# Performance work log

Measured on AMD Instinct MI355X. Metric: run time of the kernel, lower is better.

## Reference

```python
import jax, jax.numpy as jnp
import numpy as np

N_NODES = 400
HID = 96
DEC = 64
FEAT_STATIC = 8
FEAT = FEAT_STATIC + N_NODES  # 408
EPS = 1e-8


def prelu(x, a):
    # single-parameter PReLU (torch default num_parameters=1)
    return jnp.where(x >= 0, x, a * x)


def setup_inputs() -> dict:
    key = jax.random.key(0)
    ks = jax.random.split(key, 16)
    B = 16
    E = N_NODES * (N_NODES - 1) // 2  # 79800

    x = jax.random.normal(ks[0], (B, E), dtype=jnp.float32)
    node_features = jax.random.normal(ks[1], (B, N_NODES, FEAT_STATIC), dtype=jnp.float32)
    sc_matrix = jax.random.uniform(ks[2], (B, N_NODES, N_NODES), dtype=jnp.float32)

    # normalization buffers (computed from train split in torch; random stand-ins)
    static_mean = jax.random.normal(ks[3], (1, 1, FEAT_STATIC), dtype=jnp.float32) * 0.1
    static_std = jnp.ones((1, 1, FEAT_STATIC), dtype=jnp.float32)

    def lin(k, fin, fout):
        kw, kb = jax.random.split(k)
        lim = 1.0 / np.sqrt(fin)
        W = jax.random.uniform(kw, (fin, fout), minval=-lim, maxval=lim, dtype=jnp.float32)
        b = jax.random.uniform(kb, (fout,), minval=-lim, maxval=lim, dtype=jnp.float32)
        return W, b

    W_e1, b_e1 = lin(ks[4], FEAT, HID)
    W_e2, b_e2 = lin(ks[5], HID, HID)
    W_d1, b_d1 = lin(ks[6], 3 * HID, DEC)  # symmetric decoder: 3 * node_embed_dim
    W_d2, b_d2 = lin(ks[7], DEC, DEC)
    W_d3, b_d3 = lin(ks[8], DEC, 1)

    a25 = jnp.float32(0.25)

    ei_np, ej_np = np.triu_indices(N_NODES, k=1)
    ei = jnp.asarray(ei_np, dtype=jnp.int32)
    ej = jnp.asarray(ej_np, dtype=jnp.int32)

    return {
        "x": x, "node_features": node_features, "sc_matrix": sc_matrix,
        "static_mean": static_mean, "static_std": static_std,
        "W_e1": W_e1, "b_e1": b_e1, "a_e1": a25,
        "W_e2": W_e2, "b_e2": b_e2, "a_e2": a25,
        "W_d1": W_d1, "b_d1": b_d1, "a_d1": a25,
        "W_d2": W_d2, "b_d2": b_d2, "a_d2": a25,
        "W_d3": W_d3, "b_d3": b_d3,
        "ei": ei, "ej": ej,
    }


def reference(x, node_features, sc_matrix, static_mean, static_std,
              W_e1, b_e1, a_e1, W_e2, b_e2, a_e2,
              W_d1, b_d1, a_d1, W_d2, b_d2, a_d2, W_d3, b_d3, ei, ej):
    # x (SC upper triangle) is only used for batch size in the torch module.
    # static anatomical block: z-score with train stats
    s = (node_features - static_mean) / (static_std + EPS)  # [B,N,8]
    # sc_row block, 'brain_scale': divide by per-matrix mean
    m = sc_matrix / jnp.maximum(
        jnp.mean(sc_matrix, axis=(-2, -1), keepdims=True), EPS)  # [B,N,N]
    feats = jnp.concatenate([s, m], axis=-1)  # [B,N,408]

    # shared node encoder (dropout inactive at eval)
    h = prelu(feats @ W_e1 + b_e1, a_e1)
    h = prelu(h @ W_e2 + b_e2, a_e2)  # [B,N,96]

    # per-edge gather over upper-triangle indices
    h_i = h[:, ei, :]  # [B,E,96]
    h_j = h[:, ej, :]
    # symmetric edge features
    edge_feat = jnp.concatenate(
        [h_i + h_j, jnp.abs(h_i - h_j), h_i * h_j], axis=-1)  # [B,E,288]

    z = prelu(edge_feat @ W_d1 + b_d1, a_d1)
    z = prelu(z @ W_d2 + b_d2, a_d2)
    out = (z @ W_d3 + b_d3)[..., 0]  # [B,E]
    return out
```

## Files before the change

kernel.cpp:

```cpp
#include <hip/hip_runtime.h>

#define NN 400
#define HID 96
#define EDGES 79800
#define BATCH 16
#define ROWS (BATCH*EDGES)
#define NT 13
#define NPAIRS 91

typedef _Float16 f16;
typedef f16 f16x2 __attribute__((ext_vector_type(2)));
typedef f16 f16x8 __attribute__((ext_vector_type(8)));
typedef __fp16 fp16x2 __attribute__((ext_vector_type(2)));
typedef float f32x16 __attribute__((ext_vector_type(16)));
typedef unsigned int u32;
typedef unsigned long long u64;

union H8 { f16x8 h; u32 u[4]; f16x2 p[4]; fp16x2 q[4]; u64 d[2]; };
union C2 { f16x2 h; fp16x2 q; u32 u; };

__device__ inline f16x2 pkrtz(float a, float b) {
  C2 c; c.q = __builtin_amdgcn_cvt_pkrtz(a, b); return c.h;
}
__device__ inline u32 pkrtz_u(float a, float b) {
  C2 c; c.q = __builtin_amdgcn_cvt_pkrtz(a, b); return c.u;
}
__device__ inline float fdot2a(f16x2 a, f16x2 b, float c) {
#if __has_builtin(__builtin_amdgcn_fdot2)
  C2 ca, cb; ca.h = a; cb.h = b;
  return __builtin_amdgcn_fdot2(ca.q, cb.q, c, false);
#else
  return c + (float)a.x*(float)b.x + (float)a.y*(float)b.y;
#endif
}

__device__ inline f16x8 habs8(f16x8 x) {
  H8 t; t.h = x;
  t.u[0] &= 0x7fff7fffu; t.u[1] &= 0x7fff7fffu;
  t.u[2] &= 0x7fff7fffu; t.u[3] &= 0x7fff7fffu;
  return t.h;
}

__device__ inline f16x8 pack8(float a0,float a1,float a2,float a3,
                              float a4,float a5,float a6,float a7){
  H8 u;
  u.p[0] = pkrtz(a0,a1);
  u.p[1] = pkrtz(a2,a3);
  u.p[2] = pkrtz(a4,a5);
  u.p[3] = pkrtz(a6,a7);
  return u.h;
}

__global__ void prep_mean_kernel(const float* __restrict__ We1, const float* __restrict__ We2,
                                 const float* __restrict__ W1, const float* __restrict__ W2,
                                 const float* __restrict__ sc,
                                 u32* __restrict__ wq, float* __restrict__ mpart) {
  if (blockIdx.x >= 140) {
    int p = blockIdx.x - 140;
    int b = p >> 4, part = p & 15;
    const float4* src = (const float4*)(sc + (size_t)b*160000) + part*2500;
    float s = 0.f;
    for (int i = threadIdx.x; i < 2500; i += 256) {
      float4 v = src[i];
      s += (v.x + v.y) + (v.z + v.w);
    }
    __shared__ float red[256];
    red[threadIdx.x] = s; __syncthreads();
    for (int off = 128; off > 0; off >>= 1) {
      if (threadIdx.x < off) red[threadIdx.x] += red[threadIdx.x + off];
      __syncthreads();
    }
    if (threadIdx.x == 0) mpart[p] = red[0];
    return;
  }
  int D = blockIdx.x*256 + threadIdx.x;
  float v0, v1;
  if (D < 9216) {
    int frag = D >> 8;  int t = frag >> 1, q = frag & 1;
    int rem = D & 255;  int lane = rem >> 2, dj = rem & 3;
    int c = lane & 31, h2 = lane >> 5;
    int k = 16*t + 8*h2 + 2*dj;
    int d = 32*q + c;
    v0 = W1[k*64 + d]; v1 = W1[(k+1)*64 + d];
  } else if (D < 11264) {
    int Dl = D - 9216;
    int frag = Dl >> 8; int t2 = frag >> 1, q = frag & 1;
    int rem = Dl & 255; int lane = rem >> 2, dj = rem & 3;
    int c = lane & 31, h2 = lane >> 5;
    int p = 8*t2 + 4*h2 + dj;
    int d = 32*q + c;
    v0 = W2[p*64 + d]; v1 = W2[(p+32)*64 + d];
  } else if (D < 31232) {
    int Dl = D - 11264;
    int frag = Dl >> 8; int t = frag/3, ct = frag - 3*t;
    int rem = Dl & 255; int lane = rem >> 2, dj = rem & 3;
    int c = lane & 31, h2 = lane >> 5;
    int k0 = 16*t + 8*h2 + 2*dj, k1 = k0 + 1;
    int d = 32*ct + c;
    v0 = (k0 < 400) ? We1[(8+k0)*96 + d] : (k0 < 408 ? We1[(k0-400)*96 + d] : 0.f);
    v1 = (k1 < 400) ? We1[(8+k1)*96 + d] : (k1 < 408 ? We1[(k1-400)*96 + d] : 0.f);
  } else {
    int Dl = D - 31232;
    int frag = Dl >> 8; int t = frag/3, ct = frag - 3*t;
    int rem = Dl & 255; int lane = rem >> 2, dj = rem & 3;
    int c = lane & 31, h2 = lane >> 5;
    int k = 16*t + 8*h2 + 2*dj;
    int d = 32*ct + c;
    v0 = We2[k*96 + d]; v1 = We2[(k+1)*96 + d];
  }
  wq[D] = pkrtz_u(v0, v1);
}

__global__ __launch_bounds__(256) void enc_kernel(
    const float* __restrict__ sc, const float* __restrict__ nf,
    const float* __restrict__ smean, const float* __restrict__ sstd,
    const float* __restrict__ be1, const float* __restrict__ ae1,
    const float* __restrict__ be2, const float* __restrict__ ae2,
    const float* __restrict__ mpart, const u32* __restrict__ wq,
    f16* __restrict__ hout) {
  __shared__ u32 lds[12288 + 1664];
  const int tid = threadIdx.x;
  const int wid = tid >> 6, lane = tid & 63;
  const int c = lane & 31, h2 = lane >> 5;
  const int r0 = blockIdx.x * 32;
  {
    int row = tid >> 3, seg = tid & 7;
    int r = r0 + row;
    int b = r / 400;
    float ms = 0.f;
    const float4* mp4 = (const float4*)(mpart + 16*b);
#pragma unroll
    for (int k = 0; k < 4; ++k) { float4 v = mp4[k]; ms += (v.x+v.y)+(v.z+v.w); }
    float rm = 1.f / fmaxf(ms*(1.f/160000.f), 1e-8f);
    const float4* src = (const float4*)(sc + (size_t)r*400);
#pragma unroll
    for (int i = 0; i < 13; ++i) {
      int col4 = seg + 8*i;
      if (col4 < 100) {
        float4 v = src[col4];
        u32 lo = pkrtz_u(v.x*rm, v.y*rm);
        u32 hi = pkrtz_u(v.z*rm, v.w*rm);
        *(u64*)(lds + row*210 + col4*2) = (u64)lo | ((u64)hi << 32);
      }
    }
  }
  __syncthreads();
  int tb = (wid==0) ? 0 : (wid==1) ? 7 : (wid==2) ? 14 : 20;
  int te = (wid==0) ? 7 : (wid==1) ? 14 : (wid==2) ? 20 : 26;
  f32x16 acc[3] = {};
  const u32* wb1 = wq + 11264;
  for (int t = tb; t < te; ++t) {
    f16x8 af;
    if (t < 25) {
      H8 av;
      const u32* ap = lds + c*210 + 8*t + 4*h2;
      av.d[0] = *(const u64*)ap;
      av.d[1] = *(const u64*)(ap + 2);
      af = av.h;
    } else {
      af = (f16x8){};
      if (h2 == 0) {
        int r = r0 + c;
        float q0[8];
#pragma unroll
        for (int j = 0; j < 8; ++j)
          q0[j] = (nf[r*8 + j] - smean[j]) / (sstd[j] + 1e-8f);
        af = pack8(q0[0],q0[1],q0[2],q0[3],q0[4],q0[5],q0[6],q0[7]);
      }
    }
#pragma unroll
    for (int ct = 0; ct < 3; ++ct) {
      f16x8 bf = *(const f16x8*)(wb1 + ((t*3+ct)*64 + lane)*4);
      acc[ct] = __builtin_amdgcn_mfma_f32_32x32x16_f16(af, bf, acc[ct], 0,0,0);
    }
  }
  __syncthreads();
#pragma unroll
  for (int ct = 0; ct < 3; ++ct) {
    union { f32x16 v; float4 f[4]; } u; u.v = acc[ct];
#pragma unroll
    for (int i4 = 0; i4 < 4; ++i4)
      *(float4*)(lds + (((wid*3+ct)*4 + i4)*64 + lane)*4) = u.f[i4];
  }
  __syncthreads();
  f16* zb16 = (f16*)(lds + 12288);
  const float a1 = *ae1;
  if (wid < 3) {
    float bv = be1[32*wid + c];
    f32x16 s;
#pragma unroll
    for (int i = 0; i < 16; ++i) s[i] = bv;
#pragma unroll
    for (int w2 = 0; w2 < 4; ++w2) {
#pragma unroll
      for (int i4 = 0; i4 < 4; ++i4) {
        float4 f = *(const float4*)(lds + (((w2*3+wid)*4 + i4)*64 + lane)*4);
        s[4*i4+0] += f.x; s[4*i4+1] += f.y; s[4*i4+2] += f.z; s[4*i4+3] += f.w;
      }
    }
#pragma unroll
    for (int r = 0; r < 16; ++r) {
      float v = s[r]; v = fmaxf(v, a1*v);
      int row = (r & 3) + 8*(r >> 2) + 4*h2;
      zb16[row*104 + 32*wid + c] = (f16)v;
    }
  }
  __syncthreads();
  if (wid < 3) {
    const float a2 = *ae2;
    float bv = be2[32*wid + c];
    f32x16 acc2;
#pragma unroll
    for (int i = 0; i < 16; ++i) acc2[i] = bv;
    const u32* wb2 = wq + 31232;
#pragma unroll
    for (int t = 0; t < 6; ++t) {
      f16x8 af = *(const f16x8*)(zb16 + c*104 + 16*t + 8*h2);
      f16x8 bf = *(const f16x8*)(wb2 + ((t*3+wid)*64 + lane)*4);
      acc2 = __builtin_amdgcn_mfma_f32_32x32x16_f16(af, bf, acc2, 0,0,0);
    }
#pragma unroll
    for (int rr = 0; rr < 16; ++rr) {
      int row = (rr & 3) + 8*(rr >> 2) + 4*h2;
      float v = acc2[rr]; v = fmaxf(v, a2*v);
      hout[(r0 + row)*96 + 32*wid + c] = (f16)v;
    }
  }
}

__global__ __launch_bounds__(256, 2) void decoder_kernel(
    const f16* __restrict__ hbuf, const u32* __restrict__ wq,
    const float* __restrict__ b1, const float* __restrict__ b2,
    const float* __restrict__ ad1, const float* __restrict__ ad2,
    const float* __restrict__ W3, const float* __restrict__ b3p,
    float* __restrict__ out) {
  __shared__ alignas(16) u32 smem[15872];
  const int tid = threadIdx.x;
  int p = blockIdx.x;
  int b = p / NPAIRS, pr = p - b*NPAIRS;
  int I = 0;
  while (pr >= NT - I) { pr -= NT - I; ++I; }
  const int J = I + pr;
  {
    int r = tid >> 2;
    int side = r >> 5, rr = r & 31;
    int nb = (side ? J : I)*32 + rr;
    nb = nb < NN ? nb : NN-1;
    const float4* src = (const float4*)(hbuf + (size_t)(b*NN + nb)*HID) + (tid & 3)*3;
    float4* dst = (float4*)(smem + side*1536 + rr*48) + (tid & 3)*3;
    dst[0] = src[0]; dst[1] = src[1]; dst[2] = src[2];
  }
  {
    float4* dst = (float4*)(smem + 3072);
    const float4* srcw = (const float4*)wq;
    for (int i = tid; i < 2048; i += 256) dst[i] = srcw[i];
  }
  __syncthreads();

  const int lane = tid & 63;
  const int wid  = tid >> 6;
  const int c = lane & 31, h2 = lane >> 5;
  const f16* hI16 = (const f16*)smem;
  const f16* hJrow = (const f16*)(smem + 1536) + c*HID;
  const f16* wfr = (const f16*)(smem + 3072);
  u32* zb = smem + 11264 + wid*1152;
  f16x8 bp4[2], bp5[2];
  bp4[0] = *(const f16x8*)(wq + ((32+0)*64 + lane)*4);
  bp4[1] = *(const f16x8*)(wq + ((32+1)*64 + lane)*4);
  bp5[0] = *(const f16x8*)(wq + ((34+0)*64 + lane)*4);
  bp5[1] = *(const f16x8*)(wq + ((34+1)*64 + lane)*4);
  f16x8 w2f[4][2];
#pragma unroll
  for (int t2 = 0; t2 < 4; ++t2) {
    w2f[t2][0] = *(const f16x8*)(wq + 9216 + ((t2*2+0)*64 + lane)*4);
    w2f[t2][1] = *(const f16x8*)(wq + 9216 + ((t2*2+1)*64 + lane)*4);
  }
  const float b1x = b1[c], b1y = b1[c+32];
  const float b2x = b2[c], b2y = b2[c+32];
  const float a1 = *ad1, a2 = *ad2, b3 = *b3p;
  const f16x2 a1v = pkrtz(a1, a1);
  const f16x2 a2v = pkrtz(a2, a2);
  const f16x2 w3p = pkrtz(W3[c], W3[c+32]);
  const f16x2 ones2 = pkrtz(1.f, 1.f);
  const int gj = J*32 + c;
  const int bofs = b*EDGES;

  for (int it = 0; it < 4; ++it) {
    const int i0 = it*8 + wid*2;
    const f16* hi0 = hI16 + (i0+0)*HID;
    const f16* hi1 = hI16 + (i0+1)*HID;
    f32x16 acc[2][2];
#pragma unroll
    for (int r = 0; r < 16; ++r) {
      acc[0][0][r] = b1x; acc[0][1][r] = b1y;
      acc[1][0][r] = b1x; acc[1][1][r] = b1y;
    }
#pragma unroll
    for (int t = 0; t < 6; ++t) {
      f16x8 bs0 = *(const f16x8*)(wfr + (((t   )*2+0)*64 + lane)*8);
      f16x8 bs1 = *(const f16x8*)(wfr + (((t   )*2+1)*64 + lane)*8);
      f16x8 bd0 = *(const f16x8*)(wfr + (((t+ 6)*2+0)*64 + lane)*8);
      f16x8 bd1 = *(const f16x8*)(wfr + (((t+ 6)*2+1)*64 + lane)*8);
      f16x8 bp0 = (t < 4) ? *(const f16x8*)(wfr + (((t+12)*2+0)*64 + lane)*8)
                          : (t == 4 ? bp4[0] : bp5[0]);
      f16x8 bp1 = (t < 4) ? *(const f16x8*)(wfr + (((t+12)*2+1)*64 + lane)*8)
                          : (t == 4 ? bp4[1] : bp5[1]);
      f16x8 hj = *(const f16x8*)(hJrow + 16*t + 8*h2);
#pragma unroll
      for (int m = 0; m < 2; ++m) {
        f16x8 hi = *(const f16x8*)((m ? hi1 : hi0) + 16*t + 8*h2);
        f16x8 su = hi + hj;
        f16x8 di = habs8(hi - hj);
        f16x8 prd = hi * hj;
        acc[m][0] = __builtin_amdgcn_mfma_f32_32x32x16_f16(su, bs0, acc[m][0], 0,0,0);
        acc[m][1] = __builtin_amdgcn_mfma_f32_32x32x16_f16(su, bs1, acc[m][1], 0,0,0);
        acc[m][0] = __builtin_amdgcn_mfma_f32_32x32x16_f16(di, bd0, acc[m][0], 0,0,0);
        acc[m][1] = __builtin_amdgcn_mfma_f32_32x32x16_f16(di, bd1, acc[m][1], 0,0,0);
        acc[m][0] = __builtin_amdgcn_mfma_f32_32x32x16_f16(prd, bp0, acc[m][0], 0,0,0);
        acc[m][1] = __builtin_amdgcn_mfma_f32_32x32x16_f16(prd, bp1, acc[m][1], 0,0,0);
      }
    }
#pragma unroll
    for (int m = 0; m < 2; ++m) {
#pragma unroll
      for (int r = 0; r < 16; ++r) {
        f16x2 pz = pkrtz(acc[m][0][r], acc[m][1][r]);
        pz = __builtin_elementwise_max(pz, pz * a1v);
        C2 cv; cv.h = pz;
        int row = (r & 3) + 8*(r >> 2) + 4*h2;
        zb[row*36 + c] = cv.u;
      }
      f16x8 za[4];
#pragma unroll
      for (int t2 = 0; t2 < 4; ++t2)
        za[t2] = *(const f16x8*)((const f16*)zb + (c*36 + 8*t2 + 4*h2)*2);
      f32x16 zacc[2];
#pragma unroll
      for (int r = 0; r < 16; ++r) { zacc[0][r] = b2x; zacc[1][r] = b2y; }
#pragma unroll
      for (int t2 = 0; t2 < 4; ++t2) {
        zacc[0] = __builtin_amdgcn_mfma_f32_32x32x16_f16(za[t2], w2f[t2][0], zacc[0], 0,0,0);
        zacc[1] = __builtin_amdgcn_mfma_f32_32x32x16_f16(za[t2], w2f[t2][1], zacc[1], 0,0,0);
      }
#pragma unroll
      for (int r = 0; r < 16; ++r) {
        f16x2 pz = pkrtz(zacc[0][r], zacc[1][r]);
        pz = __builtin_elementwise_max(pz, pz * a2v);
        pz = pz * w3p;
        C2 cv; cv.h = pz;
        int row = (r & 3) + 8*(r >> 2) + 4*h2;
        zb[row*36 + c] = cv.u;
      }
      float ssum = 0.f;
#pragma unroll
      for (int g = 0; g < 4; ++g) {
        H8 v; v.h = *(const f16x8*)((const f16*)zb + (c*36 + 16*h2 + 4*g)*2);
#pragma unroll
        for (int dw = 0; dw < 4; ++dw)
          ssum = fdot2a(v.p[dw], ones2, ssum);
      }
      ssum += __shfl_xor(ssum, 32);
      int gi = I*32 + i0 + m;
      bool valid = (gi < gj) && (gj < NN);
      if (h2 == 0 && valid) {
        int eo = bofs + gi*(799 - gi)/2 + (gj - gi - 1);
        out[eo] = ssum + b3;
      }
    }
  }
}

extern "C" void kernel_launch(void* const* d_in, const int* in_sizes, int n_in,
                              void* d_out, int out_size, void* d_ws, size_t ws_size,
                              hipStream_t stream) {
  const float* nf  = (const float*)d_in[1];
  const float* sc  = (const float*)d_in[2];
  const float* sm  = (const float*)d_in[3];
  const float* ss  = (const float*)d_in[4];
  const float* We1 = (const float*)d_in[5];
  const float* be1 = (const float*)d_in[6];
  const float* ae1 = (const float*)d_in[7];
  const float* We2 = (const float*)d_in[8];
  const float* be2 = (const float*)d_in[9];
  const float* ae2 = (const float*)d_in[10];
  const float* W1  = (const float*)d_in[11];
  const float* b1  = (const float*)d_in[12];
  const float* a1  = (const float*)d_in[13];
  const float* W2  = (const float*)d_in[14];
  const float* b2  = (const float*)d_in[15];
  const float* a2  = (const float*)d_in[16];
  const float* W3  = (const float*)d_in[17];
  const float* b3  = (const float*)d_in[18];
  float* out = (float*)d_out;

  char* ws = (char*)d_ws;
  float* mpart = (float*)ws;
  f16*   hbuf = (f16*)(ws + 1024);
  u32*   wq   = (u32*)(ws + 1024 + 1228800);

  prep_mean_kernel<<<396, 256, 0, stream>>>(We1, We2, W1, W2, sc, wq, mpart);
  enc_kernel<<<200, 256, 0, stream>>>(sc, nf, sm, ss, be1, ae1, be2, ae2,
                                      mpart, wq, hbuf);
  decoder_kernel<<<BATCH*NPAIRS, 256, 0, stream>>>(hbuf, wq, b1, b2, a1, a2,
                                                   W3, b3, out);
}
```

Before: 184.7 us.

## Transpose decoder MFMAs to keep intermediates in registers via permlane32 swap

Swaps the MFMA operand roles so weights become the A operand and edge features the B operand. The layer-1 output then feeds layer 2 straight from registers using permlane32_swap, replacing the LDS round-trip through a per-wave z buffer. The layer-3 dot product is done in registers against prepacked W3 pairs. Biases are injected through an extra rank-1 MFMA, the J-side node rows are loaded directly into registers, and W2 moves into LDS. Shared memory shrinks, so launch bounds rise to 3 blocks per CU, at the cost of extra MFMAs and higher register pressure.

Measured after the change: 353.7 us. 91.5% more time.

```diff
diff --git a/kernel.cpp b/kernel.cpp
--- a/kernel.cpp
+++ b/kernel.cpp
@@ -49,6 +49,11 @@
   u.p[2] = pkrtz(a4,a5);
   u.p[3] = pkrtz(a6,a7);
   return u.h;
+}
+
+__device__ inline void plswap(u32 &x, u32 &y) {
+  auto r = __builtin_amdgcn_permlane32_swap((int)x, (int)y, false, false);
+  x = (u32)r[0]; y = (u32)r[1];
 }
 
 __global__ void prep_mean_kernel(const float* __restrict__ We1, const float* __restrict__ We2,
@@ -87,9 +92,9 @@
     int frag = Dl >> 8; int t2 = frag >> 1, q = frag & 1;
     int rem = Dl & 255; int lane = rem >> 2, dj = rem & 3;
     int c = lane & 31, h2 = lane >> 5;
-    int p = 8*t2 + 4*h2 + dj;
+    int k = 16*t2 + 8*h2 + 2*dj;
     int d = 32*q + c;
-    v0 = W2[p*64 + d]; v1 = W2[(p+32)*64 + d];
+    v0 = W2[k*64 + d]; v1 = W2[(k+1)*64 + d];
   } else if (D < 31232) {
     int Dl = D - 11264;
     int frag = Dl >> 8; int t = frag/3, ct = frag - 3*t;
@@ -228,141 +233,138 @@
   }
 }
 
-__global__ __launch_bounds__(256, 2) void decoder_kernel(
+__global__ __launch_bounds__(256, 3) void decoder_kernel(
     const f16* __restrict__ hbuf, const u32* __restrict__ wq,
     const float* __restrict__ b1, const float* __restrict__ b2,
     const float* __restrict__ ad1, const float* __restrict__ ad2,
     const float* __restrict__ W3, const float* __restrict__ b3p,
     float* __restrict__ out) {
-  __shared__ alignas(16) u32 smem[15872];
+  __shared__ alignas(16) u32 smem[12800];
   const int tid = threadIdx.x;
   int p = blockIdx.x;
   int b = p / NPAIRS, pr = p - b*NPAIRS;
   int I = 0;
   while (pr >= NT - I) { pr -= NT - I; ++I; }
   const int J = I + pr;
+  for (int i = tid; i < 384; i += 256) {
+    int row = i / 12, off = i - row*12;
+    int nb = I*32 + row; nb = nb < NN ? nb : NN-1;
+    const float4* src = (const float4*)(hbuf + (size_t)(b*NN + nb)*HID) + off;
+    *((float4*)(smem + row*48) + off) = *src;
+  }
   {
-    int r = tid >> 2;
-    int side = r >> 5, rr = r & 31;
-    int nb = (side ? J : I)*32 + rr;
-    nb = nb < NN ? nb : NN-1;
-    const float4* src = (const float4*)(hbuf + (size_t)(b*NN + nb)*HID) + (tid & 3)*3;
-    float4* dst = (float4*)(smem + side*1536 + rr*48) + (tid & 3)*3;
-    dst[0] = src[0]; dst[1] = src[1]; dst[2] = src[2];
-  }
-  {
-    float4* dst = (float4*)(smem + 3072);
+    float4* dst = (float4*)(smem + 1536);
     const float4* srcw = (const float4*)wq;
-    for (int i = tid; i < 2048; i += 256) dst[i] = srcw[i];
-  }
-  __syncthreads();
+    for (int i = tid; i < 2816; i += 256) dst[i] = srcw[i];
+  }
 
   const int lane = tid & 63;
   const int wid  = tid >> 6;
   const int c = lane & 31, h2 = lane >> 5;
-  const f16* hI16 = (const f16*)smem;
-  const f16* hJrow = (const f16*)(smem + 1536) + c*HID;
-  const f16* wfr = (const f16*)(smem + 3072);
-  u32* zb = smem + 11264 + wid*1152;
-  f16x8 bp4[2], bp5[2];
-  bp4[0] = *(const f16x8*)(wq + ((32+0)*64 + lane)*4);
-  bp4[1] = *(const f16x8*)(wq + ((32+1)*64 + lane)*4);
-  bp5[0] = *(const f16x8*)(wq + ((34+0)*64 + lane)*4);
-  bp5[1] = *(const f16x8*)(wq + ((34+1)*64 + lane)*4);
-  f16x8 w2f[4][2];
-#pragma unroll
-  for (int t2 = 0; t2 < 4; ++t2) {
-    w2f[t2][0] = *(const f16x8*)(wq + 9216 + ((t2*2+0)*64 + lane)*4);
-    w2f[t2][1] = *(const f16x8*)(wq + 9216 + ((t2*2+1)*64 + lane)*4);
-  }
-  const float b1x = b1[c], b1y = b1[c+32];
-  const float b2x = b2[c], b2y = b2[c+32];
+  const int gj = J*32 + c;
+  const int gjc = gj < NN ? gj : NN-1;
+  f16x8 hjr[6];
+  {
+    const f16* hjp = hbuf + (size_t)(b*NN + gjc)*HID + 8*h2;
+#pragma unroll
+    for (int t = 0; t < 6; ++t) hjr[t] = *(const f16x8*)(hjp + 16*t);
+  }
   const float a1 = *ad1, a2 = *ad2, b3 = *b3p;
   const f16x2 a1v = pkrtz(a1, a1);
   const f16x2 a2v = pkrtz(a2, a2);
-  const f16x2 w3p = pkrtz(W3[c], W3[c+32]);
-  const f16x2 ones2 = pkrtz(1.f, 1.f);
-  const int gj = J*32 + c;
+  f16x8 bcst = (f16x8){};
+  f16x8 ab1f[2]; ab1f[0] = (f16x8){}; ab1f[1] = (f16x8){};
+  f16x8 ab2f[2]; ab2f[0] = (f16x8){}; ab2f[1] = (f16x8){};
+  if (h2 == 0) {
+    bcst[0] = (f16)1.f;
+    ab1f[0][0] = (f16)b1[c];      ab1f[1][0] = (f16)b1[32 + c];
+    ab2f[0][0] = (f16)b2[c];      ab2f[1][0] = (f16)b2[32 + c];
+  }
+  f16x2 w3q[2][8];
+#pragma unroll
+  for (int q2 = 0; q2 < 2; ++q2)
+#pragma unroll
+    for (int a = 0; a < 8; ++a) {
+      int base = 32*q2 + 8*(a >> 1) + 2*(a & 1) + 4*h2;
+      w3q[q2][a] = pkrtz(W3[base], W3[base + 1]);
+    }
+  __syncthreads();
+
+  const f16* hIb = (const f16*)smem;
+  const u32* wfr = smem + 1536;
+  const u32* w2a = smem + 10752;
   const int bofs = b*EDGES;
 
   for (int it = 0; it < 4; ++it) {
     const int i0 = it*8 + wid*2;
-    const f16* hi0 = hI16 + (i0+0)*HID;
-    const f16* hi1 = hI16 + (i0+1)*HID;
-    f32x16 acc[2][2];
-#pragma unroll
-    for (int r = 0; r < 16; ++r) {
-      acc[0][0][r] = b1x; acc[0][1][r] = b1y;
-      acc[1][0][r] = b1x; acc[1][1][r] = b1y;
+    f32x16 acc[2][2] = {};
+#pragma unroll
+    for (int m = 0; m < 2; ++m) {
+      acc[m][0] = __builtin_amdgcn_mfma_f32_32x32x16_f16(ab1f[0], bcst, acc[m][0], 0,0,0);
+      acc[m][1] = __builtin_amdgcn_mfma_f32_32x32x16_f16(ab1f[1], bcst, acc[m][1], 0,0,0);
     }
 #pragma unroll
     for (int t = 0; t < 6; ++t) {
-      f16x8 bs0 = *(const f16x8*)(wfr + (((t   )*2+0)*64 + lane)*8);
-      f16x8 bs1 = *(const f16x8*)(wfr + (((t   )*2+1)*64 + lane)*8);
-      f16x8 bd0 = *(const f16x8*)(wfr + (((t+ 6)*2+0)*64 + lane)*8);
-      f16x8 bd1 = *(const f16x8*)(wfr + (((t+ 6)*2+1)*64 + lane)*8);
-      f16x8 bp0 = (t < 4) ? *(const f16x8*)(wfr + (((t+12)*2+0)*64 + lane)*8)
-                          : (t == 4 ? bp4[0] : bp5[0]);
-      f16x8 bp1 = (t < 4) ? *(const f16x8*)(wfr + (((t+12)*2+1)*64 + lane)*8)
-                          : (t == 4 ? bp4[1] : bp5[1]);
-      f16x8 hj = *(const f16x8*)(hJrow + 16*t + 8*h2);
+      f16x8 as0 = *(const f16x8*)(wfr + (((t    )*2+0)*64 + lane)*4);
+      f16x8 as1 = *(const f16x8*)(wfr + (((t    )*2+1)*64 + lane)*4);
+      f16x8 ad0 = *(const f16x8*)(wfr + (((t+ 6)*2+0)*64 + lane)*4);
+      f16x8 ad1_ = *(const f16x8*)(wfr + (((t+ 6)*2+1)*64 + lane)*4);
+      f16x8 ap0 = *(const f16x8*)(wfr + (((t+12)*2+0)*64 + lane)*4);
+      f16x8 ap1 = *(const f16x8*)(wfr + (((t+12)*2+1)*64 + lane)*4);
+      f16x8 hj8 = hjr[t];
 #pragma unroll
       for (int m = 0; m < 2; ++m) {
-        f16x8 hi = *(const f16x8*)((m ? hi1 : hi0) + 16*t + 8*h2);
-        f16x8 su = hi + hj;
-        f16x8 di = habs8(hi - hj);
-        f16x8 prd = hi * hj;
-        acc[m][0] = __builtin_amdgcn_mfma_f32_32x32x16_f16(su, bs0, acc[m][0], 0,0,0);
-        acc[m][1] = __builtin_amdgcn_mfma_f32_32x32x16_f16(su, bs1, acc[m][1], 0,0,0);
-        acc[m][0] = __builtin_amdgcn_mfma_f32_32x32x16_f16(di, bd0, acc[m][0], 0,0,0);
-        acc[m][1] = __builtin_amdgcn_mfma_f32_32x32x16_f16(di, bd1, acc[m][1], 0,0,0);
-        acc[m][0] = __builtin_amdgcn_mfma_f32_32x32x16_f16(prd, bp0, acc[m][0], 0,0,0);
-        acc[m][1] = __builtin_amdgcn_mfma_f32_32x32x16_f16(prd, bp1, acc[m][1], 0,0,0);
+        f16x8 hi8 = *(const f16x8*)(hIb + (i0+m)*HID + 16*t + 8*h2);
+        f16x8 su = hi8 + hj8;
+        f16x8 di = habs8(hi8 - hj8);
+        f16x8 prd = hi8 * hj8;
+        acc[m][0] = __builtin_amdgcn_mfma_f32_32x32x16_f16(as0, su,  acc[m][0], 0,0,0);
+        acc[m][1] = __builtin_amdgcn_mfma_f32_32x32x16_f16(as1, su,  acc[m][1], 0,0,0);
+        acc[m][0] = __builtin_amdgcn_mfma_f32_32x32x16_f16(ad0, di,  acc[m][0], 0,0,0);
+        acc[m][1] = __builtin_amdgcn_mfma_f32_32x32x16_f16(ad1_, di, acc[m][1], 0,0,0);
+        acc[m][0] = __builtin_amdgcn_mfma_f32_32x32x16_f16(ap0, prd, acc[m][0], 0,0,0);
+        acc[m][1] = __builtin_amdgcn_mfma_f32_32x32x16_f16(ap1, prd, acc[m][1], 0,0,0);
       }
     }
 #pragma unroll
     for (int m = 0; m < 2; ++m) {
-#pragma unroll
-      for (int r = 0; r < 16; ++r) {
-        f16x2 pz = pkrtz(acc[m][0][r], acc[m][1][r]);
-        pz = __builtin_elementwise_max(pz, pz * a1v);
-        C2 cv; cv.h = pz;
-        int row = (r & 3) + 8*(r >> 2) + 4*h2;
-        zb[row*36 + c] = cv.u;
-      }
-      f16x8 za[4];
-#pragma unroll
-      for (int t2 = 0; t2 < 4; ++t2)
-        za[t2] = *(const f16x8*)((const f16*)zb + (c*36 + 8*t2 + 4*h2)*2);
-      f32x16 zacc[2];
-#pragma unroll
-      for (int r = 0; r < 16; ++r) { zacc[0][r] = b2x; zacc[1][r] = b2y; }
+      u32 w[16];
+#pragma unroll
+      for (int q = 0; q < 2; ++q)
+#pragma unroll
+        for (int a = 0; a < 8; ++a) {
+          f16x2 pz = pkrtz(acc[m][q][2*a], acc[m][q][2*a+1]);
+          pz = __builtin_elementwise_max(pz, pz * a1v);
+          C2 cv; cv.h = pz; w[q*8 + a] = cv.u;
+        }
+#pragma unroll
+      for (int g = 0; g < 4; ++g) {
+        plswap(w[g*4+0], w[g*4+2]);
+        plswap(w[g*4+1], w[g*4+3]);
+      }
+      f32x16 zacc[2] = {};
+      zacc[0] = __builtin_amdgcn_mfma_f32_32x32x16_f16(ab2f[0], bcst, zacc[0], 0,0,0);
+      zacc[1] = __builtin_amdgcn_mfma_f32_32x32x16_f16(ab2f[1], bcst, zacc[1], 0,0,0);
 #pragma unroll
       for (int t2 = 0; t2 < 4; ++t2) {
-        zacc[0] = __builtin_amdgcn_mfma_f32_32x32x16_f16(za[t2], w2f[t2][0], zacc[0], 0,0,0);
-        zacc[1] = __builtin_amdgcn_mfma_f32_32x32x16_f16(za[t2], w2f[t2][1], zacc[1], 0,0,0);
-      }
-#pragma unroll
-      for (int r = 0; r < 16; ++r) {
-        f16x2 pz = pkrtz(zacc[0][r], zacc[1][r]);
-        pz = __builtin_elementwise_max(pz, pz * a2v);
-        pz = pz * w3p;
-        C2 cv; cv.h = pz;
-        int row = (r & 3) + 8*(r >> 2) + 4*h2;
-        zb[row*36 + c] = cv.u;
+        H8 zf; zf.u[0] = w[4*t2]; zf.u[1] = w[4*t2+1]; zf.u[2] = w[4*t2+2]; zf.u[3] = w[4*t2+3];
+        f16x8 w20 = *(const f16x8*)(w2a + ((t2*2+0)*64 + lane)*4);
+        f16x8 w21 = *(const f16x8*)(w2a + ((t2*2+1)*64 + lane)*4);
+        zacc[0] = __builtin_amdgcn_mfma_f32_32x32x16_f16(w20, zf.h, zacc[0], 0,0,0);
+        zacc[1] = __builtin_amdgcn_mfma_f32_32x32x16_f16(w21, zf.h, zacc[1], 0,0,0);
       }
       float ssum = 0.f;
 #pragma unroll
-      for (int g = 0; g < 4; ++g) {
-        H8 v; v.h = *(const f16x8*)((const f16*)zb + (c*36 + 16*h2 + 4*g)*2);
-#pragma unroll
-        for (int dw = 0; dw < 4; ++dw)
-          ssum = fdot2a(v.p[dw], ones2, ssum);
-      }
+      for (int q2 = 0; q2 < 2; ++q2)
+#pragma unroll
+        for (int a = 0; a < 8; ++a) {
+          f16x2 pz = pkrtz(zacc[q2][2*a], zacc[q2][2*a+1]);
+          pz = __builtin_elementwise_max(pz, pz * a2v);
+          ssum = fdot2a(pz, w3q[q2][a], ssum);
+        }
       ssum += __shfl_xor(ssum, 32);
       int gi = I*32 + i0 + m;
-      bool valid = (gi < gj) && (gj < NN);
-      if (h2 == 0 && valid) {
+      if (h2 == 0 && gi < gj && gj < NN) {
         int eo = bofs + gi*(799 - gi)/2 + (gj - gi - 1);
         out[eo] = ssum + b3;
       }
```
